# Kernel optimization log

Hardware: AMD Instinct MI355X
Metric: run time of the kernel (lower is better)

The kernel has to match this reference:

```python
import jax, jax.numpy as jnp
import numpy as np

# Module scale: T timesteps, N nodes, E directed edges
T, N, E = 6, 20000, 320000
IN_F, HID, OUT_F, K = 11, 64, 3, 2  # K=2 Chebyshev graph conv


def setup_inputs() -> dict:
    key = jax.random.key(0)
    ks = jax.random.split(key, 8)
    X_seq = jax.random.normal(ks[0], (T, N, IN_F), dtype=jnp.float32)
    # col 6 is physical time; make it a monotone ramp so dt != 0 between steps
    X_seq = X_seq.at[:, :, 6].set(jnp.arange(T, dtype=jnp.float32)[:, None] * 0.01)
    edge = jax.random.randint(ks[1], (2, E), 0, N)
    s = 0.05
    # 6 ChebConvs inside GConvGRU, stacked by gate order (z, r, h)
    Wx = jax.random.normal(ks[2], (3, K, IN_F, HID), dtype=jnp.float32) * s
    Wh = jax.random.normal(ks[3], (3, K, HID, HID), dtype=jnp.float32) * s
    bx = jax.random.normal(ks[4], (3, HID), dtype=jnp.float32) * s
    bh = jax.random.normal(ks[5], (3, HID), dtype=jnp.float32) * s
    head_W = jax.random.normal(ks[6], (HID, OUT_F), dtype=jnp.float32) * s
    head_b = jnp.zeros((OUT_F,), dtype=jnp.float32)
    return dict(X_seq=X_seq, edge=edge, Wx=Wx, bx=bx, Wh=Wh, bh=bh,
                head_W=head_W, head_b=head_b)


def _cheb(x, W, b, src, dst, ew, n):
    # PyG ChebConv (sym norm, lambda_max=2): Lhat = -D^-1/2 A D^-1/2
    # K=2: out = T0(x) @ W0 + T1(x) @ W1 + b, T0 = x, T1 = Lhat x
    out = x @ W[0]
    Tx1 = jax.ops.segment_sum(ew[:, None] * x[src], dst, num_segments=n)  # [N, F]
    return out + Tx1 @ W[1] + b


def _forward(X_seq, edge, Wx, bx, Wh, bh, head_W, head_b):
    n = X_seq.shape[1]
    src, dst = edge[0], edge[1]
    deg = jax.ops.segment_sum(jnp.ones((edge.shape[1],), X_seq.dtype), src,
                              num_segments=n)
    dis = jnp.where(deg > 0, jax.lax.rsqrt(jnp.maximum(deg, 1.0)), 0.0)
    ew = -dis[src] * dis[dst]  # scaled Laplacian edge weights

    def cell(x, h):  # GConvGRU cell
        Z = jax.nn.sigmoid(_cheb(x, Wx[0], bx[0], src, dst, ew, n)
                           + _cheb(h, Wh[0], bh[0], src, dst, ew, n))
        R = jax.nn.sigmoid(_cheb(x, Wx[1], bx[1], src, dst, ew, n)
                           + _cheb(h, Wh[1], bh[1], src, dst, ew, n))
        Ht = jnp.tanh(_cheb(x, Wx[2], bx[2], src, dst, ew, n)
                      + _cheb(h * R, Wh[2], bh[2], src, dst, ew, n))
        return Z * h + (1.0 - Z) * Ht

    X_prev = jnp.concatenate([X_seq[:1], X_seq[:-1]], axis=0)

    def step(carry, xs):
        h, u_prev = carry  # u_prev is detached (stop_gradient) like u.detach()
        x_t, x_pm1, t = xs
        dt = x_t[:, 6] - x_pm1[:, 6]
        dt = jnp.where(t == 0, jnp.ones_like(dt), dt)  # guard; t=0 branch discarded
        v = (u_prev - x_pm1[:, 3:6]) / dt[:, None]
        x_mod = x_t.at[:, 3:6].set(u_prev).at[:, 8:11].set(v)
        x_in = jnp.where(t == 0, x_t, x_mod)
        h = cell(x_in, h)
        u = h @ head_W + head_b
        return (h, jax.lax.stop_gradient(u)), u

    h0 = jnp.zeros((n, Wh.shape[-1]), X_seq.dtype)
    u0 = jnp.zeros((n, head_W.shape[-1]), X_seq.dtype)
    ts = jnp.arange(X_seq.shape[0])
    _, outs = jax.lax.scan(step, (h0, u0), (X_seq, X_prev, ts))
    return outs  # [T, N, out_f]


def reference(X_seq, edge, Wx, bx, Wh, bh, head_W, head_b):
    return _forward(X_seq, edge, Wx, bx, Wh, bh, head_W, head_b)
```

## Files before the change

kernel.cpp:

```cpp
#include <hip/hip_runtime.h>
#include <hip/hip_fp16.h>
#include <math.h>

#define TSTEPS 6
#define NN 20000
#define NE 320000
#define INF 11
#define XPAD 16
#define HID 64
#define OUTF 3
#define NPW 4
#define EPMAX (NE + 7 * NN)
#define NB ((NN + 255) / 256)

__device__ __forceinline__ float bcast(float v, int l) {
    return __uint_as_float(__builtin_amdgcn_readlane(__float_as_uint(v), l));
}

__device__ __forceinline__ float tanh_safe(float a) {
    float e2 = __expf(-2.0f * fabsf(a));
    float t = (1.0f - e2) / (1.0f + e2);
    return copysignf(t, a);
}


__global__ void k_cnt(const int* __restrict__ src, const int* __restrict__ dst,
                      int* __restrict__ degi, int* __restrict__ indeg, int E) {
    int e = blockIdx.x * blockDim.x + threadIdx.x;
    if (e >= E) return;
    atomicAdd(&degi[src[e]], 1);
    atomicAdd(&indeg[dst[e]], 1);
}

__global__ __launch_bounds__(256) void k_scanA(const int* __restrict__ indeg,
                                               int* __restrict__ part,
                                               int* __restrict__ bsum, int n) {
    int idx = blockIdx.x * 256 + threadIdx.x;
    int lane = threadIdx.x & 63, wv = threadIdx.x >> 6;
    int v = (idx < n) ? ((indeg[idx] + 7) & ~7) : 0;
#pragma unroll
    for (int off = 1; off < 64; off <<= 1) {
        int t = __shfl_up(v, off);
        if (lane >= off) v += t;
    }
    __shared__ int wsum[4];
    if (lane == 63) wsum[wv] = v;
    __syncthreads();
    int add = 0;
    for (int w = 0; w < wv; ++w) add += wsum[w];
    v += add;
    if (idx < n) part[idx] = v;
    if (threadIdx.x == 255) bsum[blockIdx.x] = v;
}

__global__ __launch_bounds__(128) void k_scanB(const int* __restrict__ bsum,
                                               int* __restrict__ boff, int nb) {
    int tid = threadIdx.x;
    int lane = tid & 63, wv = tid >> 6;
    int orig = (tid < nb) ? bsum[tid] : 0;
    int v = orig;
#pragma unroll
    for (int off = 1; off < 64; off <<= 1) {
        int t = __shfl_up(v, off);
        if (lane >= off) v += t;
    }
    __shared__ int w0;
    if (lane == 63 && wv == 0) w0 = v;
    __syncthreads();
    if (wv == 1) v += w0;
    if (tid < nb) boff[tid] = v - orig;
}

__global__ __launch_bounds__(256) void k_scanC(const int* __restrict__ indeg,
                                               int* __restrict__ part,
                                               const int* __restrict__ boff,
                                               int* __restrict__ cursor, int n) {
    int idx = blockIdx.x * 256 + threadIdx.x;
    if (idx >= n) return;
    int pd = (indeg[idx] + 7) & ~7;
    int incl = part[idx] + boff[blockIdx.x];
    int excl = incl - pd;
    part[idx] = excl;
    cursor[idx] = excl;
    if (idx == n - 1) part[n] = incl;
}

__global__ void k_fill(const int* __restrict__ src, const int* __restrict__ dst,
                       const int* __restrict__ degi, int* __restrict__ cursor,
                       int2* __restrict__ pack, int E) {
    int e = blockIdx.x * blockDim.x + threadIdx.x;
    if (e >= E) return;
    int s = src[e], d = dst[e];
    float ds = (float)degi[s];
    float dd = (float)degi[d];
    float ns = ds > 0.0f ? rsqrtf(fmaxf(ds, 1.0f)) : 0.0f;
    float nd = dd > 0.0f ? rsqrtf(fmaxf(dd, 1.0f)) : 0.0f;
    int pos = atomicAdd(&cursor[d], 1);
    int2 v;
    v.x = s;
    v.y = __float_as_int(-ns * nd);
    pack[pos] = v;
}

__global__ void k_init(const float* __restrict__ Wh, const float* __restrict__ Wx,
                       float4* __restrict__ Wh4, float2* __restrict__ Wh2,
                       float4* __restrict__ Wx4, float2* __restrict__ Wx2,
                       float* __restrict__ h, __half* __restrict__ h16,
                       const float* __restrict__ Xt, float* __restrict__ xin,
                       __half* __restrict__ xin16) {
    int idx = blockIdx.x * blockDim.x + threadIdx.x;
    if (idx < NN * HID) { h[idx] = 0.0f; h16[idx] = __float2half(0.0f); }
    if (idx < HID * HID) {
        int j = idx >> 6, f = idx & 63;
        float4 v4;
        v4.x = Wh[((0 * 2 + 0) * HID + j) * HID + f];
        v4.y = Wh[((0 * 2 + 1) * HID + j) * HID + f];
        v4.z = Wh[((1 * 2 + 0) * HID + j) * HID + f];
        v4.w = Wh[((1 * 2 + 1) * HID + j) * HID + f];
        Wh4[idx] = v4;
        float2 v2;
        v2.x = Wh[((2 * 2 + 0) * HID + j) * HID + f];
        v2.y = Wh[((2 * 2 + 1) * HID + j) * HID + f];
        Wh2[idx] = v2;
    } else if (idx < HID * HID + INF * HID) {
        int k = idx - HID * HID;
        int i = k >> 6, f = k & 63;
        float4 v4;
        v4.x = Wx[((0 * 2 + 0) * INF + i) * HID + f];
        v4.y = Wx[((0 * 2 + 1) * INF + i) * HID + f];
        v4.z = Wx[((1 * 2 + 0) * INF + i) * HID + f];
        v4.w = Wx[((1 * 2 + 1) * INF + i) * HID + f];
        Wx4[k] = v4;
        float2 v2;
        v2.x = Wx[((2 * 2 + 0) * INF + i) * HID + f];
        v2.y = Wx[((2 * 2 + 1) * INF + i) * HID + f];
        Wx2[k] = v2;
    }
    if (idx < NN) {
        const float* xt = Xt + (size_t)idx * INF;
        float* xo = xin + (size_t)idx * XPAD;
        __half* xh = xin16 + (size_t)idx * XPAD;
#pragma unroll
        for (int k = 0; k < INF; ++k) { float v = xt[k]; xo[k] = v; xh[k] = __float2half(v); }
#pragma unroll
        for (int k = INF; k < XPAD; ++k) { xo[k] = 0.0f; xh[k] = __float2half(0.0f); }
    }
}


__global__ __launch_bounds__(256) void k_gz(
    const int* __restrict__ rowstart, const int2* __restrict__ pack,
    const float* __restrict__ xin, const __half* __restrict__ xin16,
    const __half* __restrict__ h16,
    const float4* __restrict__ Wx4, const float* __restrict__ bx,
    const float4* __restrict__ Wh4, const float* __restrict__ bh,
    float* __restrict__ t1x, __half* __restrict__ Zb16,
    __half* __restrict__ hr16, int n) {
    int wid = __builtin_amdgcn_readfirstlane(
        (int)((blockIdx.x * blockDim.x + threadIdx.x) >> 6));
    int wbase = wid * NPW;
    int lane = threadIdx.x & 63;
    int f16i = lane & 15, eo = lane >> 4;
    if (wbase >= n) return;

    int ps[NPW], es[NPW];
    float A0[NPW], A1[NPW], C0[NPW], C1[NPW];
    float thg[NPW], axv[NPW], hv[NPW];
#pragma unroll
    for (int nn = 0; nn < NPW; ++nn) {
        int node = wbase + nn;
        ps[nn] = rowstart[node];
        es[nn] = rowstart[node + 1];
        hv[nn] = __half2float(h16[(size_t)node * HID + lane]);
        A0[nn] = 0.0f; A1[nn] = 0.0f; C0[nn] = 0.0f; C1[nn] = 0.0f;
    }
    while ((ps[0] < es[0]) | (ps[1] < es[1]) | (ps[2] < es[2]) | (ps[3] < es[3])) {
#pragma unroll
        for (int nn = 0; nn < NPW; ++nn) {
            bool act = ps[nn] < es[nn];
            int q = act ? ps[nn] : 0;
            float m = act ? 1.0f : 0.0f;
            int2 q0 = pack[q],     q1 = pack[q + 1], q2 = pack[q + 2], q3 = pack[q + 3];
            int2 q4 = pack[q + 4], q5 = pack[q + 5], q6 = pack[q + 6], q7 = pack[q + 7];
            float w0 = __int_as_float(q0.y) * m, w1 = __int_as_float(q1.y) * m;
            float w2 = __int_as_float(q2.y) * m, w3 = __int_as_float(q3.y) * m;
            float w4 = __int_as_float(q4.y) * m, w5 = __int_as_float(q5.y) * m;
            float w6 = __int_as_float(q6.y) * m, w7 = __int_as_float(q7.y) * m;
            A0[nn] = fmaf(w0, __half2float(h16[(size_t)q0.x * HID + lane]), A0[nn]);
            A1[nn] = fmaf(w1, __half2float(h16[(size_t)q1.x * HID + lane]), A1[nn]);
            A0[nn] = fmaf(w2, __half2float(h16[(size_t)q2.x * HID + lane]), A0[nn]);
            A1[nn] = fmaf(w3, __half2float(h16[(size_t)q3.x * HID + lane]), A1[nn]);
            A0[nn] = fmaf(w4, __half2float(h16[(size_t)q4.x * HID + lane]), A0[nn]);
            A1[nn] = fmaf(w5, __half2float(h16[(size_t)q5.x * HID + lane]), A1[nn]);
            A0[nn] = fmaf(w6, __half2float(h16[(size_t)q6.x * HID + lane]), A0[nn]);
            A1[nn] = fmaf(w7, __half2float(h16[(size_t)q7.x * HID + lane]), A1[nn]);
            int2 x0 = pack[q + 2 * eo], x1 = pack[q + 2 * eo + 1];
            C0[nn] = fmaf(__int_as_float(x0.y) * m,
                          __half2float(xin16[(size_t)x0.x * XPAD + f16i]), C0[nn]);
            C1[nn] = fmaf(__int_as_float(x1.y) * m,
                          __half2float(xin16[(size_t)x1.x * XPAD + f16i]), C1[nn]);
            ps[nn] += 8;
        }
    }
#pragma unroll
    for (int nn = 0; nn < NPW; ++nn) {
        thg[nn] = A0[nn] + A1[nn];
        float cx = C0[nn] + C1[nn];
        cx += __shfl_down(cx, 32);
        cx += __shfl_down(cx, 16);
        axv[nn] = cx;
    }
#pragma unroll
    for (int nn = 0; nn < NPW; ++nn)
        if (lane < 16) t1x[(size_t)(wbase + nn) * XPAD + lane] = axv[nn];

    float xrow = xin[(size_t)wbase * XPAD + lane];
    float b0z = bx[0 * HID + lane] + bh[0 * HID + lane];
    float b0r = bx[1 * HID + lane] + bh[1 * HID + lane];
    float az[NPW], ar[NPW];
#pragma unroll
    for (int nn = 0; nn < NPW; ++nn) { az[nn] = b0z; ar[nn] = b0r; }
#pragma unroll
    for (int i = 0; i < INF; ++i) {
        float4 w = Wx4[i * HID + lane];
#pragma unroll
        for (int nn = 0; nn < NPW; ++nn) {
            float xv = bcast(xrow, nn * XPAD + i);
            float tv = bcast(axv[nn], i);
            az[nn] = fmaf(xv, w.x, fmaf(tv, w.y, az[nn]));
            ar[nn] = fmaf(xv, w.z, fmaf(tv, w.w, ar[nn]));
        }
    }
#pragma unroll 8
    for (int j = 0; j < HID; ++j) {
        float4 w = Wh4[j * HID + lane];
#pragma unroll
        for (int nn = 0; nn < NPW; ++nn) {
            float hj = bcast(hv[nn], j);
            float tj = bcast(thg[nn], j);
            az[nn] = fmaf(hj, w.x, fmaf(tj, w.y, az[nn]));
            ar[nn] = fmaf(hj, w.z, fmaf(tj, w.w, ar[nn]));
        }
    }
#pragma unroll
    for (int nn = 0; nn < NPW; ++nn) {
        int node = wbase + nn;
        float Z = 1.0f / (1.0f + __expf(-az[nn]));
        float R = 1.0f / (1.0f + __expf(-ar[nn]));
        Zb16[(size_t)node * HID + lane] = __float2half(Z);
        hr16[(size_t)node * HID + lane] = __float2half(hv[nn] * R);
    }
}

__global__ __launch_bounds__(256) void k_gc(
    const int* __restrict__ rowstart, const int2* __restrict__ pack,
    const float* __restrict__ xin, const float* __restrict__ t1x,
    float* __restrict__ h, __half* __restrict__ h16,
    const __half* __restrict__ hr16,
    const float2* __restrict__ Wx2, const float* __restrict__ bx,
    const float2* __restrict__ Wh2, const float* __restrict__ bh,
    const __half* __restrict__ Zb16,
    const float* __restrict__ hw, const float* __restrict__ hb,
    float* __restrict__ out,
    const float* __restrict__ Xcur, const float* __restrict__ Xnxt,
    float* __restrict__ xin_w, __half* __restrict__ xin16_w,
    int last, int n) {
    int wid = __builtin_amdgcn_readfirstlane(
        (int)((blockIdx.x * blockDim.x + threadIdx.x) >> 6));
    int wbase = wid * NPW;
    int lane = threadIdx.x & 63;
    if (wbase >= n) return;

    int ps[NPW], es[NPW];
    float A0[NPW], A1[NPW];
    float thg[NPW], hrv[NPW];
#pragma unroll
    for (int nn = 0; nn < NPW; ++nn) {
        int node = wbase + nn;
        ps[nn] = rowstart[node];
        es[nn] = rowstart[node + 1];
        hrv[nn] = __half2float(hr16[(size_t)node * HID + lane]);
        A0[nn] = 0.0f; A1[nn] = 0.0f;
    }
    while ((ps[0] < es[0]) | (ps[1] < es[1]) | (ps[2] < es[2]) | (ps[3] < es[3])) {
#pragma unroll
        for (int nn = 0; nn < NPW; ++nn) {
            bool act = ps[nn] < es[nn];
            int q = act ? ps[nn] : 0;
            float m = act ? 1.0f : 0.0f;
            int2 q0 = pack[q],     q1 = pack[q + 1], q2 = pack[q + 2], q3 = pack[q + 3];
            int2 q4 = pack[q + 4], q5 = pack[q + 5], q6 = pack[q + 6], q7 = pack[q + 7];
            A0[nn] = fmaf(__int_as_float(q0.y) * m,
                          __half2float(hr16[(size_t)q0.x * HID + lane]), A0[nn]);
            A1[nn] = fmaf(__int_as_float(q1.y) * m,
                          __half2float(hr16[(size_t)q1.x * HID + lane]), A1[nn]);
            A0[nn] = fmaf(__int_as_float(q2.y) * m,
                          __half2float(hr16[(size_t)q2.x * HID + lane]), A0[nn]);
            A1[nn] = fmaf(__int_as_float(q3.y) * m,
                          __half2float(hr16[(size_t)q3.x * HID + lane]), A1[nn]);
            A0[nn] = fmaf(__int_as_float(q4.y) * m,
                          __half2float(hr16[(size_t)q4.x * HID + lane]), A0[nn]);
            A1[nn] = fmaf(__int_as_float(q5.y) * m,
                          __half2float(hr16[(size_t)q5.x * HID + lane]), A1[nn]);
            A0[nn] = fmaf(__int_as_float(q6.y) * m,
                          __half2float(hr16[(size_t)q6.x * HID + lane]), A0[nn]);
            A1[nn] = fmaf(__int_as_float(q7.y) * m,
                          __half2float(hr16[(size_t)q7.x * HID + lane]), A1[nn]);
            ps[nn] += 8;
        }
    }
#pragma unroll
    for (int nn = 0; nn < NPW; ++nn) thg[nn] = A0[nn] + A1[nn];

    float xrow = xin[(size_t)wbase * XPAD + lane];
    float trow = t1x[(size_t)wbase * XPAD + lane];
    float b0 = bx[2 * HID + lane] + bh[2 * HID + lane];
    float ah[NPW];
#pragma unroll
    for (int nn = 0; nn < NPW; ++nn) ah[nn] = b0;
#pragma unroll
    for (int i = 0; i < INF; ++i) {
        float2 w = Wx2[i * HID + lane];
#pragma unroll
        for (int nn = 0; nn < NPW; ++nn) {
            float xv = bcast(xrow, nn * XPAD + i);
            float tv = bcast(trow, nn * XPAD + i);
            ah[nn] = fmaf(xv, w.x, fmaf(tv, w.y, ah[nn]));
        }
    }
#pragma unroll 8
    for (int j = 0; j < HID; ++j) {
        float2 w = Wh2[j * HID + lane];
#pragma unroll
        for (int nn = 0; nn < NPW; ++nn) {
            float hj = bcast(hrv[nn], j);
            float tj = bcast(thg[nn], j);
            ah[nn] = fmaf(hj, w.x, fmaf(tj, w.y, ah[nn]));
        }
    }
#pragma unroll
    for (int nn = 0; nn < NPW; ++nn) {
        int node = wbase + nn;
        float Ht = tanh_safe(ah[nn]);
        float z = __half2float(Zb16[(size_t)node * HID + lane]);
        float hvv = h[(size_t)node * HID + lane];
        float hnew = z * hvv + (1.0f - z) * Ht;
        h[(size_t)node * HID + lane] = hnew;
        h16[(size_t)node * HID + lane] = __float2half(hnew);
        float u0, u1, u2;
        {
            float v0 = hnew * hw[lane * OUTF + 0];
            float v1 = hnew * hw[lane * OUTF + 1];
            float v2 = hnew * hw[lane * OUTF + 2];
            for (int off = 32; off; off >>= 1) {
                v0 += __shfl_down(v0, off);
                v1 += __shfl_down(v1, off);
                v2 += __shfl_down(v2, off);
            }
            u0 = bcast(v0, 0) + hb[0];
            u1 = bcast(v1, 0) + hb[1];
            u2 = bcast(v2, 0) + hb[2];
        }
        if (lane == 0) {
            float* o = out + (size_t)node * OUTF;
            o[0] = u0; o[1] = u1; o[2] = u2;
        }
        if (!last) {
            const float* x1r = Xnxt + (size_t)node * INF;
            const float* x0r = Xcur + (size_t)node * INF;
            float x1 = (lane < INF) ? x1r[lane] : 0.0f;
            float x0v = (lane >= 3 && lane < 7) ? x0r[lane] : 0.0f;
            float dt = bcast(x1, 6) - bcast(x0v, 6);
            float inv = 1.0f / dt;
            float c3 = bcast(x0v, 3), c4 = bcast(x0v, 4), c5 = bcast(x0v, 5);
            float val;
            if (lane < 3) val = x1;
            else if (lane < 6) val = (lane == 3) ? u0 : (lane == 4) ? u1 : u2;
            else if (lane < 8) val = x1;
            else if (lane < 11) {
                float uu = (lane == 8) ? u0 : (lane == 9) ? u1 : u2;
                float cc = (lane == 8) ? c3 : (lane == 9) ? c4 : c5;
                val = (uu - cc) * inv;
            } else val = 0.0f;
            if (lane < XPAD) {
                xin_w[(size_t)node * XPAD + lane] = val;
                xin16_w[(size_t)node * XPAD + lane] = __float2half(val);
            }
        }
    }
}

extern "C" void kernel_launch(void* const* d_in, const int* in_sizes, int n_in,
                              void* d_out, int out_size, void* d_ws, size_t ws_size,
                              hipStream_t stream) {
    const float* X_seq = (const float*)d_in[0];
    const int* edge = (const int*)d_in[1];
    const float* Wx = (const float*)d_in[2];
    const float* bx = (const float*)d_in[3];
    const float* Wh = (const float*)d_in[4];
    const float* bh = (const float*)d_in[5];
    const float* head_W = (const float*)d_in[6];
    const float* head_b = (const float*)d_in[7];
    float* out = (float*)d_out;

    const int* src = edge;
    const int* dst = edge + NE;

    float* ws = (float*)d_ws;
    float4* Wh4g = (float4*)ws;
    float4* Wx4g = (float4*)(ws + 16384);
    float2* Wh2c = (float2*)(ws + 19200);
    float2* Wx2c = (float2*)(ws + 27392);
    float* fbase = ws + 28800;
    float* xin  = fbase;
    float* t1x  = xin + (size_t)NN * XPAD;
    float* h    = t1x + (size_t)NN * XPAD;
    int* degi     = (int*)(h + (size_t)NN * HID);
    int* indeg    = degi + NN;
    int* rowstart = indeg + NN;
    int* cursor   = rowstart + NN + 2;
    int* bsum     = cursor + NN;
    int* boff     = bsum + 128;
    int2* pack    = (int2*)(boff + 128);
    __half* h16   = (__half*)(pack + EPMAX);
    __half* hr16  = h16 + (size_t)NN * HID;
    __half* Zb16  = hr16 + (size_t)NN * HID;
    __half* xin16 = Zb16 + (size_t)NN * HID;

    hipMemsetAsync(degi, 0, 2 * NN * sizeof(int), stream);
    hipMemsetAsync(pack, 0, (size_t)EPMAX * sizeof(int2), stream);
    k_cnt<<<(NE + 255) / 256, 256, 0, stream>>>(src, dst, degi, indeg, NE);
    k_scanA<<<NB, 256, 0, stream>>>(indeg, rowstart, bsum, NN);
    k_scanB<<<1, 128, 0, stream>>>(bsum, boff, NB);
    k_scanC<<<NB, 256, 0, stream>>>(indeg, rowstart, boff, cursor, NN);
    k_fill<<<(NE + 255) / 256, 256, 0, stream>>>(src, dst, degi, cursor, pack, NE);
    k_init<<<(NN * HID + 255) / 256, 256, 0, stream>>>(
        Wh, Wx, Wh4g, Wh2c, Wx4g, Wx2c, h, h16, X_seq, xin, xin16);

    const int fused_grid = (NN + 4 * NPW - 1) / (4 * NPW);

    for (int t = 0; t < TSTEPS; ++t) {
        k_gz<<<fused_grid, 256, 0, stream>>>(rowstart, pack, xin, xin16, h16,
                                             Wx4g, bx, Wh4g, bh,
                                             t1x, Zb16, hr16, NN);

        const float* Xcur = X_seq + (size_t)t * NN * INF;
        const float* Xnxt = (t + 1 < TSTEPS) ? X_seq + (size_t)(t + 1) * NN * INF : X_seq;
        k_gc<<<fused_grid, 256, 0, stream>>>(rowstart, pack, xin, t1x, h, h16, hr16,
                                             Wx2c, bx, Wh2c, bh, Zb16,
                                             head_W, head_b,
                                             out + (size_t)t * NN * OUTF,
                                             Xcur, Xnxt, xin, xin16,
                                             (t + 1 == TSTEPS) ? 1 : 0, NN);
    }
}
```

Measured before the change: 434.5 us.

## Fuse timestep loop into a persistent cooperative kernel with grid syncs

Replaces the per-timestep pair of gate kernels with a single cooperative persistent kernel of 1000 blocks. Each wave owns five fixed nodes and keeps their hidden state and Z gate in registers across all timesteps, using grid.sync between the gather phases. This removes twelve kernel launches and their tail gaps, plus the Z and fp32 h round-trips through global memory. In exchange it relies on every block being co-resident, uses grid-wide barriers, and fixes the work split at five nodes per wave. The old launch path remains as a fallback if the occupancy check or the cooperative launch fails.

After: 435.0 us. No clear change (+0.1%).

```diff
diff --git a/kernel.cpp b/kernel.cpp
--- a/kernel.cpp
+++ b/kernel.cpp
@@ -1,6 +1,9 @@
 #include <hip/hip_runtime.h>
 #include <hip/hip_fp16.h>
+#include <hip/hip_cooperative_groups.h>
 #include <math.h>
+
+namespace cg = cooperative_groups;
 
 #define TSTEPS 6
 #define NN 20000
@@ -10,6 +13,8 @@
 #define HID 64
 #define OUTF 3
 #define NPW 4
+#define CNPW 5
+#define CNBLK 1000
 #define EPMAX (NE + 7 * NN)
 #define NB ((NN + 255) / 256)
 
@@ -390,6 +395,254 @@
     }
 }
 
+__global__ __launch_bounds__(256, 4) void k_loop(
+    const int* __restrict__ rowstart, const int2* __restrict__ pack,
+    const float* __restrict__ X_seq,
+    float* __restrict__ xin, __half* __restrict__ xin16,
+    __half* __restrict__ h16, __half* __restrict__ hr16,
+    float* __restrict__ t1x,
+    const float4* __restrict__ Wx4, const float2* __restrict__ Wx2,
+    const float* __restrict__ bx,
+    const float4* __restrict__ Wh4, const float2* __restrict__ Wh2,
+    const float* __restrict__ bh,
+    const float* __restrict__ hw, const float* __restrict__ hb,
+    float* __restrict__ out) {
+    cg::grid_group grid = cg::this_grid();
+    int wid = __builtin_amdgcn_readfirstlane(
+        (int)((blockIdx.x * blockDim.x + threadIdx.x) >> 6));
+    int wbase = wid * CNPW;
+    int lane = threadIdx.x & 63;
+    int f16i = lane & 15, eo = lane >> 4;
+
+    int ps0[CNPW], es0[CNPW];
+#pragma unroll
+    for (int nn = 0; nn < CNPW; ++nn) {
+        ps0[nn] = rowstart[wbase + nn];
+        es0[nn] = rowstart[wbase + nn + 1];
+    }
+    float h32[CNPW], zz[CNPW];
+#pragma unroll
+    for (int nn = 0; nn < CNPW; ++nn) h32[nn] = 0.0f;
+
+    for (int t = 0; t < TSTEPS; ++t) {
+        {
+            int ps[CNPW];
+            float A0[CNPW], A1[CNPW], C0[CNPW], C1[CNPW];
+#pragma unroll
+            for (int nn = 0; nn < CNPW; ++nn) {
+                ps[nn] = ps0[nn];
+                A0[nn] = 0.0f; A1[nn] = 0.0f; C0[nn] = 0.0f; C1[nn] = 0.0f;
+            }
+            while ((ps[0] < es0[0]) | (ps[1] < es0[1]) | (ps[2] < es0[2]) |
+                   (ps[3] < es0[3]) | (ps[4] < es0[4])) {
+#pragma unroll
+                for (int nn = 0; nn < CNPW; ++nn) {
+                    bool act = ps[nn] < es0[nn];
+                    int q = act ? ps[nn] : 0;
+                    float m = act ? 1.0f : 0.0f;
+                    int2 q0 = pack[q],     q1 = pack[q + 1], q2 = pack[q + 2], q3 = pack[q + 3];
+                    int2 q4 = pack[q + 4], q5 = pack[q + 5], q6 = pack[q + 6], q7 = pack[q + 7];
+                    float w0 = __int_as_float(q0.y) * m, w1 = __int_as_float(q1.y) * m;
+                    float w2 = __int_as_float(q2.y) * m, w3 = __int_as_float(q3.y) * m;
+                    float w4 = __int_as_float(q4.y) * m, w5 = __int_as_float(q5.y) * m;
+                    float w6 = __int_as_float(q6.y) * m, w7 = __int_as_float(q7.y) * m;
+                    A0[nn] = fmaf(w0, __half2float(h16[(size_t)q0.x * HID + lane]), A0[nn]);
+                    A1[nn] = fmaf(w1, __half2float(h16[(size_t)q1.x * HID + lane]), A1[nn]);
+                    A0[nn] = fmaf(w2, __half2float(h16[(size_t)q2.x * HID + lane]), A0[nn]);
+                    A1[nn] = fmaf(w3, __half2float(h16[(size_t)q3.x * HID + lane]), A1[nn]);
+                    A0[nn] = fmaf(w4, __half2float(h16[(size_t)q4.x * HID + lane]), A0[nn]);
+                    A1[nn] = fmaf(w5, __half2float(h16[(size_t)q5.x * HID + lane]), A1[nn]);
+                    A0[nn] = fmaf(w6, __half2float(h16[(size_t)q6.x * HID + lane]), A0[nn]);
+                    A1[nn] = fmaf(w7, __half2float(h16[(size_t)q7.x * HID + lane]), A1[nn]);
+                    int2 x0 = pack[q + 2 * eo], x1 = pack[q + 2 * eo + 1];
+                    C0[nn] = fmaf(__int_as_float(x0.y) * m,
+                                  __half2float(xin16[(size_t)x0.x * XPAD + f16i]), C0[nn]);
+                    C1[nn] = fmaf(__int_as_float(x1.y) * m,
+                                  __half2float(xin16[(size_t)x1.x * XPAD + f16i]), C1[nn]);
+                    ps[nn] += 8;
+                }
+            }
+            float thg[CNPW], axv[CNPW];
+#pragma unroll
+            for (int nn = 0; nn < CNPW; ++nn) {
+                thg[nn] = A0[nn] + A1[nn];
+                float cx = C0[nn] + C1[nn];
+                cx += __shfl_down(cx, 32);
+                cx += __shfl_down(cx, 16);
+                axv[nn] = cx;
+                if (lane < 16) t1x[(size_t)(wbase + nn) * XPAD + lane] = cx;
+            }
+
+            float xrow = xin[(size_t)wbase * XPAD + lane];
+            float xr4  = xin[(size_t)(wbase + 4) * XPAD + f16i];
+            float b0z = bx[0 * HID + lane] + bh[0 * HID + lane];
+            float b0r = bx[1 * HID + lane] + bh[1 * HID + lane];
+            float az[CNPW], ar[CNPW];
+#pragma unroll
+            for (int nn = 0; nn < CNPW; ++nn) { az[nn] = b0z; ar[nn] = b0r; }
+#pragma unroll
+            for (int i = 0; i < INF; ++i) {
+                float4 w = Wx4[i * HID + lane];
+#pragma unroll
+                for (int nn = 0; nn < CNPW; ++nn) {
+                    float xv = (nn < 4) ? bcast(xrow, nn * XPAD + i) : bcast(xr4, i);
+                    float tv = bcast(axv[nn], i);
+                    az[nn] = fmaf(xv, w.x, fmaf(tv, w.y, az[nn]));
+                    ar[nn] = fmaf(xv, w.z, fmaf(tv, w.w, ar[nn]));
+                }
+            }
+#pragma unroll 8
+            for (int j = 0; j < HID; ++j) {
+                float4 w = Wh4[j * HID + lane];
+#pragma unroll
+                for (int nn = 0; nn < CNPW; ++nn) {
+                    float hj = bcast(h32[nn], j);
+                    float tj = bcast(thg[nn], j);
+                    az[nn] = fmaf(hj, w.x, fmaf(tj, w.y, az[nn]));
+                    ar[nn] = fmaf(hj, w.z, fmaf(tj, w.w, ar[nn]));
+                }
+            }
+#pragma unroll
+            for (int nn = 0; nn < CNPW; ++nn) {
+                int node = wbase + nn;
+                float Z = 1.0f / (1.0f + __expf(-az[nn]));
+                float R = 1.0f / (1.0f + __expf(-ar[nn]));
+                zz[nn] = Z;
+                hr16[(size_t)node * HID + lane] = __float2half(h32[nn] * R);
+            }
+        }
+        __threadfence();
+        grid.sync();
+
+        {
+            int ps[CNPW];
+            float A0[CNPW], A1[CNPW];
+#pragma unroll
+            for (int nn = 0; nn < CNPW; ++nn) {
+                ps[nn] = ps0[nn];
+                A0[nn] = 0.0f; A1[nn] = 0.0f;
+            }
+            while ((ps[0] < es0[0]) | (ps[1] < es0[1]) | (ps[2] < es0[2]) |
+                   (ps[3] < es0[3]) | (ps[4] < es0[4])) {
+#pragma unroll
+                for (int nn = 0; nn < CNPW; ++nn) {
+                    bool act = ps[nn] < es0[nn];
+                    int q = act ? ps[nn] : 0;
+                    float m = act ? 1.0f : 0.0f;
+                    int2 q0 = pack[q],     q1 = pack[q + 1], q2 = pack[q + 2], q3 = pack[q + 3];
+                    int2 q4 = pack[q + 4], q5 = pack[q + 5], q6 = pack[q + 6], q7 = pack[q + 7];
+                    A0[nn] = fmaf(__int_as_float(q0.y) * m,
+                                  __half2float(hr16[(size_t)q0.x * HID + lane]), A0[nn]);
+                    A1[nn] = fmaf(__int_as_float(q1.y) * m,
+                                  __half2float(hr16[(size_t)q1.x * HID + lane]), A1[nn]);
+                    A0[nn] = fmaf(__int_as_float(q2.y) * m,
+                                  __half2float(hr16[(size_t)q2.x * HID + lane]), A0[nn]);
+                    A1[nn] = fmaf(__int_as_float(q3.y) * m,
+                                  __half2float(hr16[(size_t)q3.x * HID + lane]), A1[nn]);
+                    A0[nn] = fmaf(__int_as_float(q4.y) * m,
+                                  __half2float(hr16[(size_t)q4.x * HID + lane]), A0[nn]);
+                    A1[nn] = fmaf(__int_as_float(q5.y) * m,
+                                  __half2float(hr16[(size_t)q5.x * HID + lane]), A1[nn]);
+                    A0[nn] = fmaf(__int_as_float(q6.y) * m,
+                                  __half2float(hr16[(size_t)q6.x * HID + lane]), A0[nn]);
+                    A1[nn] = fmaf(__int_as_float(q7.y) * m,
+                                  __half2float(hr16[(size_t)q7.x * HID + lane]), A1[nn]);
+                    ps[nn] += 8;
+                }
+            }
+            float thg[CNPW], hrv[CNPW];
+#pragma unroll
+            for (int nn = 0; nn < CNPW; ++nn) {
+                thg[nn] = A0[nn] + A1[nn];
+                hrv[nn] = __half2float(hr16[(size_t)(wbase + nn) * HID + lane]);
+            }
+
+            float xrow = xin[(size_t)wbase * XPAD + lane];
+            float xr4  = xin[(size_t)(wbase + 4) * XPAD + f16i];
+            float trow = t1x[(size_t)wbase * XPAD + lane];
+            float tr4  = t1x[(size_t)(wbase + 4) * XPAD + f16i];
+            float b0 = bx[2 * HID + lane] + bh[2 * HID + lane];
+            float ah[CNPW];
+#pragma unroll
+            for (int nn = 0; nn < CNPW; ++nn) ah[nn] = b0;
+#pragma unroll
+            for (int i = 0; i < INF; ++i) {
+                float2 w = Wx2[i * HID + lane];
+#pragma unroll
+                for (int nn = 0; nn < CNPW; ++nn) {
+                    float xv = (nn < 4) ? bcast(xrow, nn * XPAD + i) : bcast(xr4, i);
+                    float tv = (nn < 4) ? bcast(trow, nn * XPAD + i) : bcast(tr4, i);
+                    ah[nn] = fmaf(xv, w.x, fmaf(tv, w.y, ah[nn]));
+                }
+            }
+#pragma unroll 8
+            for (int j = 0; j < HID; ++j) {
+                float2 w = Wh2[j * HID + lane];
+#pragma unroll
+                for (int nn = 0; nn < CNPW; ++nn) {
+                    float hj = bcast(hrv[nn], j);
+                    float tj = bcast(thg[nn], j);
+                    ah[nn] = fmaf(hj, w.x, fmaf(tj, w.y, ah[nn]));
+                }
+            }
+            const float* Xcur = X_seq + (size_t)t * NN * INF;
+            const float* Xnxt = X_seq + (size_t)(t + 1 < TSTEPS ? t + 1 : t) * NN * INF;
+#pragma unroll
+            for (int nn = 0; nn < CNPW; ++nn) {
+                int node = wbase + nn;
+                float Ht = tanh_safe(ah[nn]);
+                float hnew = zz[nn] * h32[nn] + (1.0f - zz[nn]) * Ht;
+                h32[nn] = hnew;
+                h16[(size_t)node * HID + lane] = __float2half(hnew);
+                float u0, u1, u2;
+                {
+                    float v0 = hnew * hw[lane * OUTF + 0];
+                    float v1 = hnew * hw[lane * OUTF + 1];
+                    float v2 = hnew * hw[lane * OUTF + 2];
+                    for (int off = 32; off; off >>= 1) {
+                        v0 += __shfl_down(v0, off);
+                        v1 += __shfl_down(v1, off);
+                        v2 += __shfl_down(v2, off);
+                    }
+                    u0 = bcast(v0, 0) + hb[0];
+                    u1 = bcast(v1, 0) + hb[1];
+                    u2 = bcast(v2, 0) + hb[2];
+                }
+                if (lane == 0) {
+                    float* o = out + (size_t)t * NN * OUTF + (size_t)node * OUTF;
+                    o[0] = u0; o[1] = u1; o[2] = u2;
+                }
+                if (t + 1 < TSTEPS) {
+                    const float* x1r = Xnxt + (size_t)node * INF;
+                    const float* x0r = Xcur + (size_t)node * INF;
+                    float x1 = (lane < INF) ? x1r[lane] : 0.0f;
+                    float x0v = (lane >= 3 && lane < 7) ? x0r[lane] : 0.0f;
+                    float dt = bcast(x1, 6) - bcast(x0v, 6);
+                    float inv = 1.0f / dt;
+                    float c3 = bcast(x0v, 3), c4 = bcast(x0v, 4), c5 = bcast(x0v, 5);
+                    float val;
+                    if (lane < 3) val = x1;
+                    else if (lane < 6) val = (lane == 3) ? u0 : (lane == 4) ? u1 : u2;
+                    else if (lane < 8) val = x1;
+                    else if (lane < 11) {
+                        float uu = (lane == 8) ? u0 : (lane == 9) ? u1 : u2;
+                        float cc = (lane == 8) ? c3 : (lane == 9) ? c4 : c5;
+                        val = (uu - cc) * inv;
+                    } else val = 0.0f;
+                    if (lane < XPAD) {
+                        xin[(size_t)node * XPAD + lane] = val;
+                        xin16[(size_t)node * XPAD + lane] = __float2half(val);
+                    }
+                }
+            }
+        }
+        if (t + 1 < TSTEPS) {
+            __threadfence();
+            grid.sync();
+        }
+    }
+}
+
 extern "C" void kernel_launch(void* const* d_in, const int* in_sizes, int n_in,
                               void* d_out, int out_size, void* d_ws, size_t ws_size,
                               hipStream_t stream) {
@@ -437,20 +690,53 @@
     k_init<<<(NN * HID + 255) / 256, 256, 0, stream>>>(
         Wh, Wx, Wh4g, Wh2c, Wx4g, Wx2c, h, h16, X_seq, xin, xin16);
 
-    const int fused_grid = (NN + 4 * NPW - 1) / (4 * NPW);
-
-    for (int t = 0; t < TSTEPS; ++t) {
-        k_gz<<<fused_grid, 256, 0, stream>>>(rowstart, pack, xin, xin16, h16,
-                                             Wx4g, bx, Wh4g, bh,
-                                             t1x, Zb16, hr16, NN);
-
-        const float* Xcur = X_seq + (size_t)t * NN * INF;
-        const float* Xnxt = (t + 1 < TSTEPS) ? X_seq + (size_t)(t + 1) * NN * INF : X_seq;
-        k_gc<<<fused_grid, 256, 0, stream>>>(rowstart, pack, xin, t1x, h, h16, hr16,
-                                             Wx2c, bx, Wh2c, bh, Zb16,
-                                             head_W, head_b,
-                                             out + (size_t)t * NN * OUTF,
-                                             Xcur, Xnxt, xin, xin16,
-                                             (t + 1 == TSTEPS) ? 1 : 0, NN);
-    }
-}
+    int maxB = 0;
+    hipError_t oe = hipOccupancyMaxActiveBlocksPerMultiprocessor(&maxB, k_loop, 256, 0);
+    bool coop_ok = (oe == hipSuccess) && (maxB * 256 >= CNBLK);
+    if (coop_ok) {
+        const int* rowstart_c = rowstart;
+        const int2* pack_c = pack;
+        const float* X_c = X_seq;
+        float* xin_c = xin;
+        __half* xin16_c = xin16;
+        __half* h16_c = h16;
+        __half* hr16_c = hr16;
+        float* t1x_c = t1x;
+        const float4* Wx4_c = Wx4g;
+        const float2* Wx2_c = Wx2c;
+        const float* bx_c = bx;
+        const float4* Wh4_c = Wh4g;
+        const float2* Wh2_c = Wh2c;
+        const float* bh_c = bh;
+        const float* hw_c = head_W;
+        const float* hb_c = head_b;
+        float* out_c = out;
+        void* kargs[] = {
+            (void*)&rowstart_c, (void*)&pack_c, (void*)&X_c,
+            (void*)&xin_c, (void*)&xin16_c, (void*)&h16_c, (void*)&hr16_c,
+            (void*)&t1x_c,
+            (void*)&Wx4_c, (void*)&Wx2_c, (void*)&bx_c,
+            (void*)&Wh4_c, (void*)&Wh2_c, (void*)&bh_c,
+            (void*)&hw_c, (void*)&hb_c, (void*)&out_c
+        };
+        hipError_t le = hipLaunchCooperativeKernel((const void*)k_loop, dim3(CNBLK),
+                                                   dim3(256), kargs, 0, stream);
+        coop_ok = (le == hipSuccess);
+    }
+    if (!coop_ok) {
+        const int fused_grid = (NN + 4 * NPW - 1) / (4 * NPW);
+        for (int t = 0; t < TSTEPS; ++t) {
+            k_gz<<<fused_grid, 256, 0, stream>>>(rowstart, pack, xin, xin16, h16,
+                                                 Wx4g, bx, Wh4g, bh,
+                                                 t1x, Zb16, hr16, NN);
+            const float* Xcur = X_seq + (size_t)t * NN * INF;
+            const float* Xnxt = (t + 1 < TSTEPS) ? X_seq + (size_t)(t + 1) * NN * INF : X_seq;
+            k_gc<<<fused_grid, 256, 0, stream>>>(rowstart, pack, xin, t1x, h, h16, hr16,
+                                                 Wx2c, bx, Wh2c, bh, Zb16,
+                                                 head_W, head_b,
+                                                 out + (size_t)t * NN * OUTF,
+                                                 Xcur, Xnxt, xin, xin16,
+                                                 (t + 1 == TSTEPS) ? 1 : 0, NN);
+        }
+    }
+}
```
